# Kernel optimization log

Hardware: AMD Instinct MI355X
Metric: run time of the kernel (lower is better)

The kernel has to match this reference:

```python
import jax, jax.numpy as jnp
import numpy as np

DIM = 4096
N_HEADS = 32
N_KV_HEADS = 8
HEAD_DIM = DIM // N_HEADS            # 128
GROUP = N_HEADS // N_KV_HEADS        # 4 heads share each kv head


def setup_inputs() -> dict:
    key = jax.random.key(0)
    k1, k2, k3, k4 = jax.random.split(key, 4)
    B, S = 2, 2048
    x = jax.random.normal(k1, (B, S, DIM), dtype=jnp.float32)
    # nn.Linear weights are [out_features, in_features]
    Wq = jax.random.normal(k2, (N_HEADS * HEAD_DIM, DIM), dtype=jnp.float32) * 0.02
    Wkv = jax.random.normal(k3, (2 * N_KV_HEADS * HEAD_DIM, DIM), dtype=jnp.float32) * 0.02
    Wo = jax.random.normal(k4, (DIM, N_HEADS * HEAD_DIM), dtype=jnp.float32) * 0.02
    return {"x": x, "Wq": Wq, "Wkv": Wkv, "Wo": Wo, "start_pos": 0}


def reference(x, Wq, Wkv, Wo, start_pos):
    B, S, _ = x.shape
    total_len = start_pos + S
    # projections (Linear: x @ W.T)
    q = (x @ Wq.T).reshape(B, S, N_HEADS, HEAD_DIM)                  # (B,S,H,D)
    kv = (x @ Wkv.T).reshape(B, S, 2 * N_KV_HEADS, HEAD_DIM)
    k, v = jnp.split(kv, 2, axis=2)                                   # (B,S,Hkv,D) each
    # cache write + read with start_pos=0 is identity on k, v (prefill)
    # inflate kv heads: repeat_interleave along head axis
    k = jnp.repeat(k, GROUP, axis=2)                                  # (B,T,H,D)
    v = jnp.repeat(v, GROUP, axis=2)
    scale = HEAD_DIM ** -0.5
    scores = jnp.einsum('bqhd,bkhd->bhqk', q, k) * scale              # (B,H,S,T)
    q_idx = jnp.arange(total_len - S, total_len)[:, None]
    k_idx = jnp.arange(total_len)[None, :]
    causal = q_idx >= k_idx                                           # (S,T)
    scores = jnp.where(causal[None, None], scores, -jnp.inf)
    probs = jax.nn.softmax(scores, axis=-1)
    attn = jnp.einsum('bhqk,bkhd->bqhd', probs, v)                    # (B,S,H,D)
    attn = attn.reshape(B, S, N_HEADS * HEAD_DIM)
    return attn @ Wo.T                                                # (B,S,dim)
```

## Files before the change

kernel.cpp:

```cpp
#include <hip/hip_runtime.h>

typedef __bf16 bf16x8 __attribute__((ext_vector_type(8)));
typedef __bf16 bf16x4 __attribute__((ext_vector_type(4)));
typedef float f32x4 __attribute__((ext_vector_type(4)));
typedef unsigned short u16;
typedef unsigned short u16x8 __attribute__((ext_vector_type(8)));

#define DIM 4096
#define NHEADS 32
#define NKV 8
#define HD 128
#define BB 2
#define SS 2048
#define MROWS (BB*SS)
#define QKVP 6144
#define QSCALE 0.08838834764831843f

#define WAIT_LGKM0 asm volatile("s_waitcnt lgkmcnt(0)" ::: "memory")
#define WAIT_VM0   asm volatile("s_waitcnt vmcnt(0)" ::: "memory")
#define WAIT_VM4   asm volatile("s_waitcnt vmcnt(4)" ::: "memory")
#define SGB0       __builtin_amdgcn_sched_barrier(0)

__device__ __forceinline__ u16 f2bf(float f) {
  unsigned int u = __float_as_uint(f);
  u += 0x7fffu + ((u >> 16) & 1u);
  return (u16)(u >> 16);
}

__device__ __forceinline__ void gload16(const void* g, void* l) {
  __builtin_amdgcn_global_load_lds(
      (const __attribute__((address_space(1))) unsigned int*)g,
      (__attribute__((address_space(3))) unsigned int*)l, 16, 0, 0);
}

__device__ __forceinline__ bf16x4 tr16(const void* p) {
  bf16x4 d;
  asm volatile("ds_read_b64_tr_b16 %0, %1"
               : "=v"(d)
               : "v"((const __attribute__((address_space(3))) u16*)p)
               : "memory");
  return d;
}

template<int CTRL>
__device__ __forceinline__ float dpp_ror(float x) {
  return __int_as_float(__builtin_amdgcn_update_dpp(
      0, __float_as_int(x), CTRL, 0xF, 0xF, false));
}
__device__ __forceinline__ float red16_max(float v) {
  v = fmaxf(v, dpp_ror<0x121>(v));
  v = fmaxf(v, dpp_ror<0x122>(v));
  v = fmaxf(v, dpp_ror<0x124>(v));
  v = fmaxf(v, dpp_ror<0x128>(v));
  return v;
}
__device__ __forceinline__ float red16_sum(float v) {
  v += dpp_ror<0x121>(v);
  v += dpp_ror<0x122>(v);
  v += dpp_ror<0x124>(v);
  v += dpp_ror<0x128>(v);
  return v;
}

__global__ __launch_bounds__(256) void f2b4_kernel(
    const float* __restrict__ xa, const float* __restrict__ xb,
    const float* __restrict__ xc, const float* __restrict__ xd,
    u16* __restrict__ oa, u16* __restrict__ ob,
    u16* __restrict__ oc, u16* __restrict__ od) {
  int i = blockIdx.x * 256 + threadIdx.x;
  const float* in; u16* out; int k;
  if (i < 2097152)      { in = xa; out = oa; k = i; }
  else if (i < 4194304) { in = xb; out = ob; k = i - 2097152; }
  else if (i < 5242880) { in = xc; out = oc; k = i - 4194304; }
  else                  { in = xd; out = od; k = i - 5242880; }
  const float4* in4 = (const float4*)in;
  float4 a = in4[2*(size_t)k];
  float4 b = in4[2*(size_t)k + 1];
  u16x8 o;
  o[0]=f2bf(a.x); o[1]=f2bf(a.y); o[2]=f2bf(a.z); o[3]=f2bf(a.w);
  o[4]=f2bf(b.x); o[5]=f2bf(b.y); o[6]=f2bf(b.z); o[7]=f2bf(b.w);
  ((u16x8*)out)[k] = o;
}

template<int OUTF32>
__global__ __launch_bounds__(512, 2) void gemm256(
    const u16* __restrict__ A, const u16* __restrict__ Bm, void* __restrict__ C,
    int M, int N, int K, int nbx, int acut, float a0, float a1) {
  __shared__ char smem[131072];

  const int t = threadIdx.x;
  const int l = t & 63, w = t >> 6;
  const int l15 = l & 15, l4 = l >> 4;
  const int wm = w >> 2, wn = w & 3;

  const int nwg = gridDim.x;
  const int cpx = nwg >> 3;
  const int sw = (blockIdx.x & 7) * cpx + (blockIdx.x >> 3);
  const int bx = sw % nbx, by = sw / nbx;
  const int row0 = by * 256, col0 = bx * 256;
  const float alpha = (col0 < acut) ? a0 : a1;

  f32x4 acc[8][4] = {};

  int ro0, ko0, ro1, ko1;
  {
    int o = t, j = o >> 3, cs = (o & 7) ^ (j & 7);
    ro0 = 2*j + (cs >> 2); ko0 = (cs & 3) * 8;
    o = t + 512; j = o >> 3; cs = (o & 7) ^ (j & 7);
    ro1 = 2*j + (cs >> 2); ko1 = (cs & 3) * 8;
  }
  const char* gA0 = (const char*)(A  + (size_t)(row0 + ro0) * K + ko0);
  const char* gA1 = (const char*)(A  + (size_t)(row0 + ro1) * K + ko1);
  const char* gB0 = (const char*)(Bm + (size_t)(col0 + ro0) * K + ko0);
  const char* gB1 = (const char*)(Bm + (size_t)(col0 + ro1) * K + ko1);

  auto stage = [&](int bsel) {
    char* Ad = (char*)smem + bsel * 16384;
    char* Bd = Ad + 65536;
    gload16(gA0, Ad + w*1024);
    gload16(gA1, Ad + 8192 + w*1024);
    gload16(gB0, Bd + w*1024);
    gload16(gB1, Bd + 8192 + w*1024);
    gA0 += 64; gA1 += 64; gB0 += 64; gB1 += 64;
  };

  int offA0, offB0;
  {
    int r = wm*128 + l15, j = r >> 1;
    int c = ((r & 1)*4 + l4) ^ (j & 7);
    offA0 = j*128 + c*16;
    r = wn*64 + l15; j = r >> 1;
    c = ((r & 1)*4 + l4) ^ (j & 7);
    offB0 = 65536 + j*128 + c*16;
  }

  struct Frags { bf16x8 a0,a1,a2,a3,a4,a5,a6,a7,b0,b1,b2,b3; };
  Frags F0, F1;

  auto loadF = [&](Frags& F, int bsel) {
    const char* Sb = (const char*)smem + bsel * 16384;
    const char* Ab = Sb + offA0;
    const char* Bb = Sb + offB0;
    F.a0 = *(const bf16x8*)(Ab);
    F.a1 = *(const bf16x8*)(Ab + 1024);
    F.a2 = *(const bf16x8*)(Ab + 2048);
    F.a3 = *(const bf16x8*)(Ab + 3072);
    F.a4 = *(const bf16x8*)(Ab + 4096);
    F.a5 = *(const bf16x8*)(Ab + 5120);
    F.a6 = *(const bf16x8*)(Ab + 6144);
    F.a7 = *(const bf16x8*)(Ab + 7168);
    F.b0 = *(const bf16x8*)(Bb);
    F.b1 = *(const bf16x8*)(Bb + 1024);
    F.b2 = *(const bf16x8*)(Bb + 2048);
    F.b3 = *(const bf16x8*)(Bb + 3072);
  };

  auto mfmaC = [&](const Frags& F) {
    __builtin_amdgcn_s_setprio(1);
    acc[0][0] = __builtin_amdgcn_mfma_f32_16x16x32_bf16(F.a0, F.b0, acc[0][0], 0, 0, 0);
    acc[0][1] = __builtin_amdgcn_mfma_f32_16x16x32_bf16(F.a0, F.b1, acc[0][1], 0, 0, 0);
    acc[0][2] = __builtin_amdgcn_mfma_f32_16x16x32_bf16(F.a0, F.b2, acc[0][2], 0, 0, 0);
    acc[0][3] = __builtin_amdgcn_mfma_f32_16x16x32_bf16(F.a0, F.b3, acc[0][3], 0, 0, 0);
    acc[1][0] = __builtin_amdgcn_mfma_f32_16x16x32_bf16(F.a1, F.b0, acc[1][0], 0, 0, 0);
    acc[1][1] = __builtin_amdgcn_mfma_f32_16x16x32_bf16(F.a1, F.b1, acc[1][1], 0, 0, 0);
    acc[1][2] = __builtin_amdgcn_mfma_f32_16x16x32_bf16(F.a1, F.b2, acc[1][2], 0, 0, 0);
    acc[1][3] = __builtin_amdgcn_mfma_f32_16x16x32_bf16(F.a1, F.b3, acc[1][3], 0, 0, 0);
    acc[2][0] = __builtin_amdgcn_mfma_f32_16x16x32_bf16(F.a2, F.b0, acc[2][0], 0, 0, 0);
    acc[2][1] = __builtin_amdgcn_mfma_f32_16x16x32_bf16(F.a2, F.b1, acc[2][1], 0, 0, 0);
    acc[2][2] = __builtin_amdgcn_mfma_f32_16x16x32_bf16(F.a2, F.b2, acc[2][2], 0, 0, 0);
    acc[2][3] = __builtin_amdgcn_mfma_f32_16x16x32_bf16(F.a2, F.b3, acc[2][3], 0, 0, 0);
    acc[3][0] = __builtin_amdgcn_mfma_f32_16x16x32_bf16(F.a3, F.b0, acc[3][0], 0, 0, 0);
    acc[3][1] = __builtin_amdgcn_mfma_f32_16x16x32_bf16(F.a3, F.b1, acc[3][1], 0, 0, 0);
    acc[3][2] = __builtin_amdgcn_mfma_f32_16x16x32_bf16(F.a3, F.b2, acc[3][2], 0, 0, 0);
    acc[3][3] = __builtin_amdgcn_mfma_f32_16x16x32_bf16(F.a3, F.b3, acc[3][3], 0, 0, 0);
    acc[4][0] = __builtin_amdgcn_mfma_f32_16x16x32_bf16(F.a4, F.b0, acc[4][0], 0, 0, 0);
    acc[4][1] = __builtin_amdgcn_mfma_f32_16x16x32_bf16(F.a4, F.b1, acc[4][1], 0, 0, 0);
    acc[4][2] = __builtin_amdgcn_mfma_f32_16x16x32_bf16(F.a4, F.b2, acc[4][2], 0, 0, 0);
    acc[4][3] = __builtin_amdgcn_mfma_f32_16x16x32_bf16(F.a4, F.b3, acc[4][3], 0, 0, 0);
    acc[5][0] = __builtin_amdgcn_mfma_f32_16x16x32_bf16(F.a5, F.b0, acc[5][0], 0, 0, 0);
    acc[5][1] = __builtin_amdgcn_mfma_f32_16x16x32_bf16(F.a5, F.b1, acc[5][1], 0, 0, 0);
    acc[5][2] = __builtin_amdgcn_mfma_f32_16x16x32_bf16(F.a5, F.b2, acc[5][2], 0, 0, 0);
    acc[5][3] = __builtin_amdgcn_mfma_f32_16x16x32_bf16(F.a5, F.b3, acc[5][3], 0, 0, 0);
    acc[6][0] = __builtin_amdgcn_mfma_f32_16x16x32_bf16(F.a6, F.b0, acc[6][0], 0, 0, 0);
    acc[6][1] = __builtin_amdgcn_mfma_f32_16x16x32_bf16(F.a6, F.b1, acc[6][1], 0, 0, 0);
    acc[6][2] = __builtin_amdgcn_mfma_f32_16x16x32_bf16(F.a6, F.b2, acc[6][2], 0, 0, 0);
    acc[6][3] = __builtin_amdgcn_mfma_f32_16x16x32_bf16(F.a6, F.b3, acc[6][3], 0, 0, 0);
    acc[7][0] = __builtin_amdgcn_mfma_f32_16x16x32_bf16(F.a7, F.b0, acc[7][0], 0, 0, 0);
    acc[7][1] = __builtin_amdgcn_mfma_f32_16x16x32_bf16(F.a7, F.b1, acc[7][1], 0, 0, 0);
    acc[7][2] = __builtin_amdgcn_mfma_f32_16x16x32_bf16(F.a7, F.b2, acc[7][2], 0, 0, 0);
    acc[7][3] = __builtin_amdgcn_mfma_f32_16x16x32_bf16(F.a7, F.b3, acc[7][3], 0, 0, 0);
    __builtin_amdgcn_s_setprio(0);
  };

  const int nt = K >> 5;

  stage(0); stage(1); stage(2);
  WAIT_VM4;
  __builtin_amdgcn_s_barrier();
  loadF(F0, 0);
  WAIT_LGKM0; SGB0;

  for (int i = 0; i < nt; i += 2) {
    {
      const bool pf = (i + 3 < nt);
      if (pf) stage((i + 3) & 3);
      if (i + 1 < nt) loadF(F1, (i + 1) & 3);
      SGB0;
      mfmaC(F0);
      SGB0;
      WAIT_LGKM0; SGB0;
      if (pf) { WAIT_VM4; } else { WAIT_VM0; }
      __builtin_amdgcn_s_barrier();
    }
    if (i + 1 < nt) {
      const bool pf = (i + 4 < nt);
      if (pf) stage((i + 4) & 3);
      if (i + 2 < nt) loadF(F0, (i + 2) & 3);
      SGB0;
      mfmaC(F1);
      SGB0;
      WAIT_LGKM0; SGB0;
      if (pf) { WAIT_VM4; } else { WAIT_VM0; }
      __builtin_amdgcn_s_barrier();
    }
  }

  #pragma unroll
  for (int mi = 0; mi < 8; ++mi) {
    #pragma unroll
    for (int ni = 0; ni < 4; ++ni) {
      #pragma unroll
      for (int r = 0; r < 4; ++r) {
        size_t rr = (size_t)(row0 + wm*128 + mi*16 + l4*4 + r);
        size_t cc = (size_t)(col0 + wn*64 + ni*16 + l15);
        float v = acc[mi][ni][r] * alpha;
        if (OUTF32) ((float*)C)[rr*(size_t)N + cc] = v;
        else        ((u16*)C)[rr*(size_t)N + cc] = f2bf(v);
      }
    }
  }
}

__global__ __launch_bounds__(256, 2) void attn_kernel(
    const u16* __restrict__ QKV,
    u16* __restrict__ O) {
  __shared__ u16 Ks[2][64*128];
  __shared__ u16 Vs[2][64*128];
  __shared__ u16 Ps[4][1024];
  const int t = threadIdx.x;
  const int l = t & 63, w = t >> 6;
  const int l15 = l & 15, l4 = l >> 4;
  const int pair = blockIdx.x, h = blockIdx.y, b = blockIdx.z;
  const int hkv = h >> 2;
  const u16* Kg = QKV + (size_t)(b*SS) * QKVP + DIM + hkv*HD;
  const u16* Vg = Kg + NKV*HD;
  u16* Pw = &Ps[w][0];

  auto stage = [&](u16* Ksb, u16* Vsb, int kv0) {
    const u16* Kr = Kg + (size_t)kv0 * QKVP;
    const u16* Vr = Vg + (size_t)kv0 * QKVP;
    #pragma unroll
    for (int i = 0; i < 4; ++i) {
      int o = i*4096 + w*1024 + l*16;
      int row = o >> 8;
      int sc = l15 ^ (row & 7);
      gload16((const char*)(Kr + (size_t)row * QKVP) + sc*16,
              (char*)Ksb + i*4096 + w*1024);
    }
    #pragma unroll
    for (int i = 0; i < 4; ++i) {
      int cb = i*4 + w;
      int kv = cb*4 + ((l & 7) >> 1);
      int d0 = ((l >> 3) << 4) + (l & 1)*8;
      gload16((const char*)(Vr + (size_t)kv * QKVP + d0),
              (char*)Vsb + cb*1024);
    }
  };

  for (int half = 0; half < 2; ++half) {
    const int qb = half ? (15 - pair) : pair;
    const int q0 = qb * 128;
    const int q0w = q0 + w*32;

    const size_t qbase = ((size_t)(b*SS + q0w)) * QKVP + h*HD;
    bf16x8 qf[2][4];
    #pragma unroll
    for (int m = 0; m < 2; ++m)
      #pragma unroll
      for (int kd = 0; kd < 4; ++kd)
        qf[m][kd] = *(const bf16x8*)&QKV[qbase + (size_t)(m*16 + l15)*QKVP + kd*32 + l4*8];

    f32x4 oacc[2][8] = {};
    float mrun[2][4], lrun[2][4];
    #pragma unroll
    for (int m = 0; m < 2; ++m)
      #pragma unroll
      for (int r = 0; r < 4; ++r) { mrun[m][r] = -1e30f; lrun[m][r] = 0.f; }

    const int nst = 2*qb + 2;
    stage(Ks[0], Vs[0], 0);
    WAIT_VM0;
    __builtin_amdgcn_s_barrier();
    SGB0;

    for (int st = 0; st < nst; ++st) {
      const int kv0 = st * 64;
      u16* Ksb = Ks[st & 1];
      u16* Vsb = Vs[st & 1];
      if (st + 1 < nst) stage(Ks[(st+1) & 1], Vs[(st+1) & 1], kv0 + 64);

      if (kv0 <= q0w + 31) {
        f32x4 sacc[2][4] = {};
        __builtin_amdgcn_s_setprio(1);
        #pragma unroll
        for (int kd = 0; kd < 4; ++kd) {
          bf16x8 kf[4];
          #pragma unroll
          for (int n = 0; n < 4; ++n) {
            int row = n*16 + l15;
            int off = (row << 8) | (((kd*4 + l4) ^ (row & 7)) << 4);
            kf[n] = *(const bf16x8*)((const char*)Ksb + off);
          }
          #pragma unroll
          for (int m = 0; m < 2; ++m)
            #pragma unroll
            for (int n = 0; n < 4; ++n)
              sacc[m][n] = __builtin_amdgcn_mfma_f32_16x16x32_bf16(qf[m][kd], kf[n], sacc[m][n], 0, 0, 0);
        }
        __builtin_amdgcn_s_setprio(0);

        if (st >= 2*qb) {
          #pragma unroll
          for (int n = 0; n < 4; ++n) {
            int ki = kv0 + n*16 + l15;
            #pragma unroll
            for (int m = 0; m < 2; ++m)
              #pragma unroll
              for (int r = 0; r < 4; ++r) {
                int qi = q0w + m*16 + l4*4 + r;
                if (ki > qi) sacc[m][n][r] = -1e30f;
              }
          }
        }

        float pr[2][4][4];
        #pragma unroll
        for (int m = 0; m < 2; ++m) {
          #pragma unroll
          for (int r = 0; r < 4; ++r) {
            float s0 = sacc[m][0][r], s1 = sacc[m][1][r];
            float s2 = sacc[m][2][r], s3 = sacc[m][3][r];
            float vm = fmaxf(fmaxf(s0, s1), fmaxf(s2, s3));
            vm = red16_max(vm);
            float mo = mrun[m][r];
            float mnew = fmaxf(mo, vm);
            float al = __expf(mo - mnew);
            float p0 = __expf(s0 - mnew), p1 = __expf(s1 - mnew);
            float p2 = __expf(s2 - mnew), p3 = __expf(s3 - mnew);
            float rs = red16_sum((p0 + p1) + (p2 + p3));
            mrun[m][r] = mnew;
            lrun[m][r] = lrun[m][r]*al + rs;
            #pragma unroll
            for (int dn = 0; dn < 8; ++dn) oacc[m][dn][r] *= al;
            pr[m][r][0] = p0; pr[m][r][1] = p1; pr[m][r][2] = p2; pr[m][r][3] = p3;
          }
        }

        #pragma unroll
        for (int kvh = 0; kvh < 2; ++kvh) {
          #pragma unroll
          for (int m = 0; m < 2; ++m)
            #pragma unroll
            for (int nn = 0; nn < 2; ++nn) {
              int n = kvh*2 + nn;
              bf16x4 w4;
              w4[0] = (__bf16)pr[m][0][n]; w4[1] = (__bf16)pr[m][1][n];
              w4[2] = (__bf16)pr[m][2][n]; w4[3] = (__bf16)pr[m][3][n];
              *(bf16x4*)((char*)Pw + ((nn*4 + (l15 >> 2))*2 + m)*128
                                   + (l15 & 3)*32 + l4*8) = w4;
            }
          const char* pb = (const char*)Pw + l4*512 + l15*8;
          bf16x4 a00 = tr16(pb);
          bf16x4 a01 = tr16(pb + 256);
          bf16x4 a10 = tr16(pb + 128);
          bf16x4 a11 = tr16(pb + 384);
          const char* vb = (const char*)Vsb + l4*2048 + l15*8 + kvh*8192;
          bf16x4 b0[8], b1[8];
          #pragma unroll
          for (int dn = 0; dn < 8; ++dn) {
            b0[dn] = tr16(vb + dn*128);
            b1[dn] = tr16(vb + dn*128 + 1024);
          }
          WAIT_LGKM0; SGB0;
          bf16x8 pa0 = __builtin_shufflevector(a00, a01, 0,1,2,3,4,5,6,7);
          bf16x8 pa1 = __builtin_shufflevector(a10, a11, 0,1,2,3,4,5,6,7);
          __builtin_amdgcn_s_setprio(1);
          #pragma unroll
          for (int dn = 0; dn < 8; ++dn) {
            bf16x8 v8 = __builtin_shufflevector(b0[dn], b1[dn], 0,1,2,3,4,5,6,7);
            oacc[0][dn] = __builtin_amdgcn_mfma_f32_16x16x32_bf16(pa0, v8, oacc[0][dn], 0, 0, 0);
            oacc[1][dn] = __builtin_amdgcn_mfma_f32_16x16x32_bf16(pa1, v8, oacc[1][dn], 0, 0, 0);
          }
          __builtin_amdgcn_s_setprio(0);
        }
      }

      WAIT_VM0;
      __builtin_amdgcn_s_barrier();
      SGB0;
    }

    const size_t obase = ((size_t)(b*SS + q0w)) * DIM + h*HD;
    #pragma unroll
    for (int m = 0; m < 2; ++m) {
      #pragma unroll
      for (int r = 0; r < 4; ++r) {
        float inv = 1.0f / lrun[m][r];
        int srow = m*16 + l4*4 + r;
        #pragma unroll
        for (int dn = 0; dn < 8; ++dn)
          O[obase + (size_t)srow*DIM + dn*16 + l15] = f2bf(oacc[m][dn][r] * inv);
      }
    }
  }
}

extern "C" void kernel_launch(void* const* d_in, const int* in_sizes, int n_in,
                              void* d_out, int out_size, void* d_ws, size_t ws_size,
                              hipStream_t stream) {
  const float* x   = (const float*)d_in[0];
  const float* Wq  = (const float*)d_in[1];
  const float* Wkv = (const float*)d_in[2];
  const float* Wo  = (const float*)d_in[3];

  if (ws_size < (160ull << 20)) return;
  char* ws = (char*)d_ws;
  u16* xb   = (u16*)(ws);
  u16* Wqb  = (u16*)(ws + (32ull  << 20));
  u16* Wkvb = (u16*)(ws + (64ull  << 20));
  u16* Wob  = (u16*)(ws + (80ull  << 20));
  u16* QKVb = (u16*)(ws + (112ull << 20));
  u16* attnb = xb;

  f2b4_kernel<<<28672, 256, 0, stream>>>(x, Wq, Wkv, Wo, xb, Wqb, Wkvb, Wob);

  gemm256<0><<<dim3(16*24), 512, 0, stream>>>(xb, Wqb, QKVb,
                                              MROWS, QKVP, DIM, 24, DIM, QSCALE, 1.0f);

  attn_kernel<<<dim3(8, NHEADS, BB), 256, 0, stream>>>(QKVb, attnb);

  gemm256<1><<<dim3(16*16), 512, 0, stream>>>(attnb, Wob, d_out,
                                              MROWS, DIM, DIM, 16, 0, 1.0f, 1.0f);
}
```

Baseline: 543.6 us.

## Shrink GEMM tile to 256x128 with 4 waves and triple-buffered LDS

The GEMM kernel now uses 256-thread blocks computing 256x128 output tiles instead of 512-thread blocks computing 256x256. The LDS ring drops from four buffers to three, cutting shared memory from 128KB to 72KB, which may allow two blocks per CU. The grid doubles to 768 and 512 blocks so more CUs stay busy and the last wave is less uneven. The cost is less data reuse per tile, so more global and L2 traffic for the B operand, and a different vmcnt wait depth.

```diff
diff --git a/kernel.cpp b/kernel.cpp
--- a/kernel.cpp
+++ b/kernel.cpp
@@ -18,7 +18,7 @@
 
 #define WAIT_LGKM0 asm volatile("s_waitcnt lgkmcnt(0)" ::: "memory")
 #define WAIT_VM0   asm volatile("s_waitcnt vmcnt(0)" ::: "memory")
-#define WAIT_VM4   asm volatile("s_waitcnt vmcnt(4)" ::: "memory")
+#define WAIT_VM6   asm volatile("s_waitcnt vmcnt(6)" ::: "memory")
 #define SGB0       __builtin_amdgcn_sched_barrier(0)
 
 __device__ __forceinline__ u16 f2bf(float f) {
@@ -83,45 +83,52 @@
 }
 
 template<int OUTF32>
-__global__ __launch_bounds__(512, 2) void gemm256(
+__global__ __launch_bounds__(256, 2) void gemm256(
     const u16* __restrict__ A, const u16* __restrict__ Bm, void* __restrict__ C,
     int M, int N, int K, int nbx, int acut, float a0, float a1) {
-  __shared__ char smem[131072];
+  __shared__ char smem[73728];
 
   const int t = threadIdx.x;
   const int l = t & 63, w = t >> 6;
   const int l15 = l & 15, l4 = l >> 4;
-  const int wm = w >> 2, wn = w & 3;
+  const int wm = w >> 1, wn = w & 1;
 
   const int nwg = gridDim.x;
   const int cpx = nwg >> 3;
   const int sw = (blockIdx.x & 7) * cpx + (blockIdx.x >> 3);
   const int bx = sw % nbx, by = sw / nbx;
-  const int row0 = by * 256, col0 = bx * 256;
+  const int row0 = by * 256, col0 = bx * 128;
   const float alpha = (col0 < acut) ? a0 : a1;
 
   f32x4 acc[8][4] = {};
 
-  int ro0, ko0, ro1, ko1;
+  const u16* pA0; const u16* pA1; const u16* pA2; const u16* pA3;
+  const u16* pB0; const u16* pB1;
   {
-    int o = t, j = o >> 3, cs = (o & 7) ^ (j & 7);
-    ro0 = 2*j + (cs >> 2); ko0 = (cs & 3) * 8;
-    o = t + 512; j = o >> 3; cs = (o & 7) ^ (j & 7);
-    ro1 = 2*j + (cs >> 2); ko1 = (cs & 3) * 8;
+    int u, j, cs, r, kc;
+    u = t;          j = u >> 3; cs = (u & 7) ^ (j & 7); r = 2*j + (cs >> 2); kc = (cs & 3)*8;
+    pA0 = A + (size_t)(row0 + r) * K + kc;
+    u = t + 256;    j = u >> 3; cs = (u & 7) ^ (j & 7); r = 2*j + (cs >> 2); kc = (cs & 3)*8;
+    pA1 = A + (size_t)(row0 + r) * K + kc;
+    u = t + 512;    j = u >> 3; cs = (u & 7) ^ (j & 7); r = 2*j + (cs >> 2); kc = (cs & 3)*8;
+    pA2 = A + (size_t)(row0 + r) * K + kc;
+    u = t + 768;    j = u >> 3; cs = (u & 7) ^ (j & 7); r = 2*j + (cs >> 2); kc = (cs & 3)*8;
+    pA3 = A + (size_t)(row0 + r) * K + kc;
+    u = t;          j = u >> 3; cs = (u & 7) ^ (j & 7); r = 2*j + (cs >> 2); kc = (cs & 3)*8;
+    pB0 = Bm + (size_t)(col0 + r) * K + kc;
+    u = t + 256;    j = u >> 3; cs = (u & 7) ^ (j & 7); r = 2*j + (cs >> 2); kc = (cs & 3)*8;
+    pB1 = Bm + (size_t)(col0 + r) * K + kc;
   }
-  const char* gA0 = (const char*)(A  + (size_t)(row0 + ro0) * K + ko0);
-  const char* gA1 = (const char*)(A  + (size_t)(row0 + ro1) * K + ko1);
-  const char* gB0 = (const char*)(Bm + (size_t)(col0 + ro0) * K + ko0);
-  const char* gB1 = (const char*)(Bm + (size_t)(col0 + ro1) * K + ko1);
-
-  auto stage = [&](int bsel) {
-    char* Ad = (char*)smem + bsel * 16384;
-    char* Bd = Ad + 65536;
-    gload16(gA0, Ad + w*1024);
-    gload16(gA1, Ad + 8192 + w*1024);
-    gload16(gB0, Bd + w*1024);
-    gload16(gB1, Bd + 8192 + w*1024);
-    gA0 += 64; gA1 += 64; gB0 += 64; gB1 += 64;
+
+  auto stage = [&](int tile, int buf) {
+    char* d = (char*)smem + buf * 24576 + w*1024;
+    const int k0 = tile * 32;
+    gload16(pA0 + k0, d);
+    gload16(pA1 + k0, d + 4096);
+    gload16(pA2 + k0, d + 8192);
+    gload16(pA3 + k0, d + 12288);
+    gload16(pB0 + k0, d + 16384);
+    gload16(pB1 + k0, d + 20480);
   };
 
   int offA0, offB0;
@@ -131,14 +138,14 @@
     offA0 = j*128 + c*16;
     r = wn*64 + l15; j = r >> 1;
     c = ((r & 1)*4 + l4) ^ (j & 7);
-    offB0 = 65536 + j*128 + c*16;
+    offB0 = 16384 + j*128 + c*16;
   }
 
   struct Frags { bf16x8 a0,a1,a2,a3,a4,a5,a6,a7,b0,b1,b2,b3; };
   Frags F0, F1;
 
-  auto loadF = [&](Frags& F, int bsel) {
-    const char* Sb = (const char*)smem + bsel * 16384;
+  auto loadF = [&](Frags& F, int buf) {
+    const char* Sb = (const char*)smem + buf * 24576;
     const char* Ab = Sb + offA0;
     const char* Bb = Sb + offB0;
     F.a0 = *(const bf16x8*)(Ab);
@@ -194,34 +201,35 @@
 
   const int nt = K >> 5;
 
-  stage(0); stage(1); stage(2);
-  WAIT_VM4;
+  stage(0, 0); stage(1, 1); stage(2, 2);
+  WAIT_VM6;
   __builtin_amdgcn_s_barrier();
   loadF(F0, 0);
   WAIT_LGKM0; SGB0;
 
+  int b3 = 0;
   for (int i = 0; i < nt; i += 2) {
     {
-      const bool pf = (i + 3 < nt);
-      if (pf) stage((i + 3) & 3);
-      if (i + 1 < nt) loadF(F1, (i + 1) & 3);
+      if (i + 3 < nt) stage(i + 3, b3);
+      const int bn = (b3 == 2) ? 0 : b3 + 1;
+      if (i + 1 < nt) loadF(F1, bn);
       SGB0;
       mfmaC(F0);
-      SGB0;
       WAIT_LGKM0; SGB0;
-      if (pf) { WAIT_VM4; } else { WAIT_VM0; }
+      if (i + 3 < nt) { WAIT_VM6; } else { WAIT_VM0; }
       __builtin_amdgcn_s_barrier();
+      b3 = bn;
     }
     if (i + 1 < nt) {
-      const bool pf = (i + 4 < nt);
-      if (pf) stage((i + 4) & 3);
-      if (i + 2 < nt) loadF(F0, (i + 2) & 3);
+      if (i + 4 < nt) stage(i + 4, b3);
+      const int bn = (b3 == 2) ? 0 : b3 + 1;
+      if (i + 2 < nt) loadF(F0, bn);
       SGB0;
       mfmaC(F1);
-      SGB0;
       WAIT_LGKM0; SGB0;
-      if (pf) { WAIT_VM4; } else { WAIT_VM0; }
+      if (i + 4 < nt) { WAIT_VM6; } else { WAIT_VM0; }
       __builtin_amdgcn_s_barrier();
+      b3 = bn;
     }
   }
 
@@ -444,11 +452,11 @@
 
   f2b4_kernel<<<28672, 256, 0, stream>>>(x, Wq, Wkv, Wo, xb, Wqb, Wkvb, Wob);
 
-  gemm256<0><<<dim3(16*24), 512, 0, stream>>>(xb, Wqb, QKVb,
-                                              MROWS, QKVP, DIM, 24, DIM, QSCALE, 1.0f);
+  gemm256<0><<<dim3(768), 256, 0, stream>>>(xb, Wqb, QKVb,
+                                            MROWS, QKVP, DIM, 48, DIM, QSCALE, 1.0f);
 
   attn_kernel<<<dim3(8, NHEADS, BB), 256, 0, stream>>>(QKVb, attnb);
 
-  gemm256<1><<<dim3(16*16), 512, 0, stream>>>(attnb, Wob, d_out,
-                                              MROWS, DIM, DIM, 16, 0, 1.0f, 1.0f);
-}
+  gemm256<1><<<dim3(512), 256, 0, stream>>>(attnb, Wob, d_out,
+                                            MROWS, DIM, DIM, 32, 0, 1.0f, 1.0f);
+}
```

Measured after the change: 541.9 us. Within noise of the previous version (-0.3%).
